# Optimization experiments

Measured on AMD Instinct MI355X. Metric: run time of the kernel, lower is better.

The kernel has to match this reference:

```python
import jax, jax.numpy as jnp
import numpy as np

EMB_DIM = 1024
NUM_HEADS = 16
SCALE_WEIGHTS = 1.0
TINY = jnp.finfo(jnp.float32).tiny


def setup_inputs() -> dict:
    key = jax.random.key(0)
    k1, k2, k3 = jax.random.split(key, 3)
    B, S = 2, 2048
    x = jax.random.normal(k1, (B, S, EMB_DIM), dtype=jnp.float32)
    weights = jax.random.uniform(k2, (B, S), dtype=jnp.float32)
    W_qkv = jax.random.normal(k3, (EMB_DIM, 3 * EMB_DIM), dtype=jnp.float32) / np.sqrt(EMB_DIM)
    b_qkv = jnp.zeros((3 * EMB_DIM,), dtype=jnp.float32)
    return {"x": x, "weights": weights, "W_qkv": W_qkv, "b_qkv": b_qkv}


def reference(x, weights, W_qkv, b_qkv):
    B, S, E = x.shape
    H = NUM_HEADS
    hd = E // H
    # QKV projection: [B,S,3E] -> [B,H,S,3*hd] -> split
    qkv = x @ W_qkv + b_qkv
    qkv = qkv.reshape(B, S, H, 3 * hd).transpose(0, 2, 1, 3)
    q, k, v = jnp.split(qkv, 3, axis=-1)  # each [B,H,S,hd]
    # weights: [B,S] -> [B,1,1,S] (broadcast over heads and query positions)
    w = weights[:, None, None, :]
    # scores with log-weight bias and hard masks
    attn_logits = jnp.einsum("bhqd,bhkd->bhqk", q, k) / jnp.sqrt(jnp.asarray(hd, x.dtype))
    attn_logits = attn_logits + jnp.log(w / SCALE_WEIGHTS + TINY)
    attn_logits = jnp.where(w == 0, -9e15, attn_logits)
    attn_logits = jnp.where(w == 1, 9e15, attn_logits)
    attention = jax.nn.softmax(attn_logits, axis=-1)
    values = jnp.einsum("bhqk,bhkd->bhqd", attention, v)
    return values.transpose(0, 2, 1, 3).reshape(B, S, E)
```

## Files before the change

### kernel.cpp

```cpp
#include <hip/hip_runtime.h>
#include <math.h>

#define B_  2
#define S_  2048
#define E_  1024
#define H_  16
#define HD_ 64
#define N3_ 3072
#define M_  (B_*S_)

typedef _Float16 h8 __attribute__((ext_vector_type(8)));
typedef _Float16 h4 __attribute__((ext_vector_type(4)));
typedef float    f4 __attribute__((ext_vector_type(4)));

__global__ void logw_kernel(const float* __restrict__ w, float* __restrict__ lw) {
    int i = blockIdx.x * blockDim.x + threadIdx.x;
    if (i < B_ * S_) {
        float x = w[i];
        float v;
        if (x == 0.0f)       v = -9.0e15f;
        else if (x == 1.0f)  v =  9.0e15f;
        else                 v = logf(x + 1.17549435e-38f);
        lw[i] = v;
    }
}

__global__ void cvt_x_kernel(const float* __restrict__ x, _Float16* __restrict__ x16) {
    int i = (blockIdx.x * 256 + threadIdx.x) * 8;
    float4 u = *(const float4*)&x[i];
    float4 v = *(const float4*)&x[i + 4];
    h8 o;
    o[0] = (_Float16)u.x; o[1] = (_Float16)u.y; o[2] = (_Float16)u.z; o[3] = (_Float16)u.w;
    o[4] = (_Float16)v.x; o[5] = (_Float16)v.y; o[6] = (_Float16)v.z; o[7] = (_Float16)v.w;
    *(h8*)&x16[i] = o;
}

__global__ __launch_bounds__(256) void transpose_w_kernel(
        const float* __restrict__ W, _Float16* __restrict__ Wt) {
    __shared__ float T[64][65];
    int k0 = blockIdx.x * 64, n0 = blockIdx.y * 64;
    int tid = threadIdx.x;
    int r = tid >> 4, c4 = (tid & 15) * 4;
#pragma unroll
    for (int i = 0; i < 4; i++) {
        int row = r + i * 16;
        float4 u = *(const float4*)&W[(size_t)(k0 + row) * N3_ + n0 + c4];
        T[c4 + 0][row] = u.x; T[c4 + 1][row] = u.y;
        T[c4 + 2][row] = u.z; T[c4 + 3][row] = u.w;
    }
    __syncthreads();
#pragma unroll
    for (int i = 0; i < 4; i++) {
        int rn = r + i * 16;
        h4 p;
        p[0] = (_Float16)T[rn][c4 + 0]; p[1] = (_Float16)T[rn][c4 + 1];
        p[2] = (_Float16)T[rn][c4 + 2]; p[3] = (_Float16)T[rn][c4 + 3];
        *(h4*)&Wt[(size_t)(n0 + rn) * E_ + k0 + c4] = p;
    }
}

__global__ __launch_bounds__(256) void qkv_gemm_f16(
        const _Float16* __restrict__ x16, const _Float16* __restrict__ wt,
        const float* __restrict__ bq,
        _Float16* __restrict__ qws, _Float16* __restrict__ kws,
        _Float16* __restrict__ vtws) {
    __shared__ _Float16 As[256 * 72];
    __shared__ _Float16 Ws[64 * 72];

    int tid = threadIdx.x;
    int wid = tid >> 6;
    int ln = tid & 15;
    int qd = (tid & 63) >> 4;
    int n0 = blockIdx.x * 64;
    int m0 = blockIdx.y * 256;
    int h = n0 / 192;
    int which = (n0 % 192) / 64;
    bool isV = (which == 2);

    f4 acc[4][4];
#pragma unroll
    for (int i = 0; i < 4; i++)
#pragma unroll
        for (int j = 0; j < 4; j++) acc[i][j] = (f4)0.0f;

    int sr = tid >> 3;
    int sc = (tid & 7) * 8;

    for (int k0 = 0; k0 < E_; k0 += 64) {
#pragma unroll
        for (int i = 0; i < 8; i++) {
            int row = sr + 32 * i;
            *(h8*)&As[row * 72 + sc] = *(const h8*)&x16[(size_t)(m0 + row) * E_ + k0 + sc];
        }
#pragma unroll
        for (int i = 0; i < 2; i++) {
            int row = sr + 32 * i;
            *(h8*)&Ws[row * 72 + sc] = *(const h8*)&wt[(size_t)(n0 + row) * E_ + k0 + sc];
        }
        __syncthreads();
#pragma unroll
        for (int ks = 0; ks < 2; ks++) {
            h8 a[4], b[4];
#pragma unroll
            for (int mt = 0; mt < 4; mt++)
                a[mt] = *(const h8*)&As[(wid * 64 + mt * 16 + ln) * 72 + ks * 32 + qd * 8];
#pragma unroll
            for (int nt = 0; nt < 4; nt++)
                b[nt] = *(const h8*)&Ws[(nt * 16 + ln) * 72 + ks * 32 + qd * 8];
            if (isV) {
#pragma unroll
                for (int i = 0; i < 4; i++)
#pragma unroll
                    for (int j = 0; j < 4; j++)
                        acc[i][j] = __builtin_amdgcn_mfma_f32_16x16x32_f16(a[i], b[j], acc[i][j], 0, 0, 0);
            } else {
#pragma unroll
                for (int i = 0; i < 4; i++)
#pragma unroll
                    for (int j = 0; j < 4; j++)
                        acc[i][j] = __builtin_amdgcn_mfma_f32_16x16x32_f16(b[i], a[j], acc[i][j], 0, 0, 0);
            }
        }
        __syncthreads();
    }

    int b = m0 >> 11;
    int bh = b * H_ + h;
    int sbase = (m0 & 2047) + wid * 64;

    if (isV) {
#pragma unroll
        for (int mt = 0; mt < 4; mt++) {
#pragma unroll
            for (int nt = 0; nt < 4; nt++) {
                int d = nt * 16 + ln;
                float bias = bq[n0 + nt * 16 + ln];
                f4 v = acc[mt][nt];
                h4 p;
                p[0] = (_Float16)(v[0] + bias); p[1] = (_Float16)(v[1] + bias);
                p[2] = (_Float16)(v[2] + bias); p[3] = (_Float16)(v[3] + bias);
                int s0 = sbase + mt * 16 + qd * 4;
                *(h4*)&vtws[((size_t)(bh * HD_ + d)) * S_ + s0] = p;
            }
        }
    } else {
        _Float16* dst = (which == 0) ? qws : kws;
        float scale = (which == 0) ? 0.125f : 1.0f;
#pragma unroll
        for (int nt = 0; nt < 4; nt++) {
            f4 bias4 = *(const f4*)&bq[n0 + nt * 16 + qd * 4];
#pragma unroll
            for (int mt = 0; mt < 4; mt++) {
                int s = sbase + mt * 16 + ln;
                f4 v = (acc[nt][mt] + bias4) * scale;
                h4 p;
                p[0] = (_Float16)v[0]; p[1] = (_Float16)v[1];
                p[2] = (_Float16)v[2]; p[3] = (_Float16)v[3];
                *(h4*)&dst[(((size_t)bh * S_ + s)) * HD_ + nt * 16 + qd * 4] = p;
            }
        }
    }
}

__global__ __launch_bounds__(256) void attn_kernel(
        const _Float16* __restrict__ q, const _Float16* __restrict__ k,
        const _Float16* __restrict__ vt, const float* __restrict__ lw,
        float* __restrict__ out) {
    __shared__ _Float16 Ks[64 * 72];
    __shared__ _Float16 Vts[64 * 72];
    __shared__ _Float16 Ps[128 * 72];
    __shared__ float lws[64];
    __shared__ float abuf[4][32];

    int tid = threadIdx.x;
    int wid = tid >> 6;
    int ln = tid & 15;
    int qd = (tid & 63) >> 4;
    int q0 = blockIdx.x * 128;
    int bh = blockIdx.y;
    int b = bh >> 4, h = bh & 15;

    const _Float16* qbase = q + (size_t)bh * S_ * HD_;
    const _Float16* kbase = k + (size_t)bh * S_ * HD_;
    const _Float16* vbase = vt + (size_t)bh * HD_ * S_;

    h8 qf[2][2];
#pragma unroll
    for (int qt = 0; qt < 2; qt++)
#pragma unroll
        for (int ds = 0; ds < 2; ds++)
            qf[qt][ds] = *(const h8*)&qbase[(size_t)(q0 + wid * 32 + qt * 16 + ln) * HD_ + ds * 32 + qd * 8];

    f4 o[2][4];
#pragma unroll
    for (int i = 0; i < 2; i++)
#pragma unroll
        for (int j = 0; j < 4; j++) o[i][j] = (f4)0.0f;
    float m_r[2] = {-INFINITY, -INFINITY};
    float l_r[2] = {0.0f, 0.0f};

    int sr = tid >> 3;
    int sc = (tid & 7) * 8;

    for (int kt = 0; kt < 32; kt++) {
        int k0 = kt * 64;
#pragma unroll
        for (int i = 0; i < 2; i++) {
            int row = sr + 32 * i;
            *(h8*)&Ks[row * 72 + sc]  = *(const h8*)&kbase[(size_t)(k0 + row) * HD_ + sc];
            *(h8*)&Vts[row * 72 + sc] = *(const h8*)&vbase[(size_t)row * S_ + k0 + sc];
        }
        if (tid < 64) lws[tid] = lw[b * S_ + k0 + tid];
        __syncthreads();

        f4 st[4][2];
#pragma unroll
        for (int i = 0; i < 4; i++)
#pragma unroll
            for (int j = 0; j < 2; j++) st[i][j] = (f4)0.0f;
#pragma unroll
        for (int ds = 0; ds < 2; ds++) {
            h8 kf[4];
#pragma unroll
            for (int i = 0; i < 4; i++)
                kf[i] = *(const h8*)&Ks[(i * 16 + ln) * 72 + ds * 32 + qd * 8];
#pragma unroll
            for (int i = 0; i < 4; i++)
#pragma unroll
                for (int qt = 0; qt < 2; qt++)
                    st[i][qt] = __builtin_amdgcn_mfma_f32_16x16x32_f16(kf[i], qf[qt][ds], st[i][qt], 0, 0, 0);
        }

        f4 lwv[4];
#pragma unroll
        for (int i = 0; i < 4; i++)
            lwv[i] = *(const f4*)&lws[i * 16 + qd * 4];
#pragma unroll
        for (int qt = 0; qt < 2; qt++) {
            float sv[16];
            float rm = -INFINITY;
#pragma unroll
            for (int i = 0; i < 4; i++)
#pragma unroll
                for (int r = 0; r < 4; r++) {
                    float v = st[i][qt][r] + lwv[i][r];
                    sv[i * 4 + r] = v;
                    rm = fmaxf(rm, v);
                }
            rm = fmaxf(rm, __shfl_xor(rm, 16));
            rm = fmaxf(rm, __shfl_xor(rm, 32));
            float mnew = fmaxf(m_r[qt], rm);
            float rs = 0.0f;
#pragma unroll
            for (int i = 0; i < 16; i++) {
                float e = __expf(sv[i] - mnew);
                sv[i] = e;
                rs += e;
            }
            rs += __shfl_xor(rs, 16);
            rs += __shfl_xor(rs, 32);
            float alpha = __expf(m_r[qt] - mnew);
            m_r[qt] = mnew;
            l_r[qt] = l_r[qt] * alpha + rs;
            if (qd == 0) abuf[wid][qt * 16 + ln] = alpha;
#pragma unroll
            for (int i = 0; i < 4; i++) {
                h4 p;
                p[0] = (_Float16)sv[i * 4 + 0]; p[1] = (_Float16)sv[i * 4 + 1];
                p[2] = (_Float16)sv[i * 4 + 2]; p[3] = (_Float16)sv[i * 4 + 3];
                *(h4*)&Ps[(wid * 32 + qt * 16 + ln) * 72 + i * 16 + qd * 4] = p;
            }
        }
        asm volatile("s_waitcnt lgkmcnt(0)" ::: "memory");

#pragma unroll
        for (int mt = 0; mt < 2; mt++) {
            f4 af = *(const f4*)&abuf[wid][mt * 16 + qd * 4];
#pragma unroll
            for (int nt = 0; nt < 4; nt++) o[mt][nt] *= af;
        }

#pragma unroll
        for (int ks = 0; ks < 2; ks++) {
            h8 pf[2], vf[4];
#pragma unroll
            for (int mt = 0; mt < 2; mt++)
                pf[mt] = *(const h8*)&Ps[(wid * 32 + mt * 16 + ln) * 72 + ks * 32 + qd * 8];
#pragma unroll
            for (int nt = 0; nt < 4; nt++)
                vf[nt] = *(const h8*)&Vts[(nt * 16 + ln) * 72 + ks * 32 + qd * 8];
#pragma unroll
            for (int mt = 0; mt < 2; mt++)
#pragma unroll
                for (int nt = 0; nt < 4; nt++)
                    o[mt][nt] = __builtin_amdgcn_mfma_f32_16x16x32_f16(pf[mt], vf[nt], o[mt][nt], 0, 0, 0);
        }
        __syncthreads();
    }

    if (qd == 0) {
        abuf[wid][ln] = l_r[0];
        abuf[wid][16 + ln] = l_r[1];
    }
    asm volatile("s_waitcnt lgkmcnt(0)" ::: "memory");
#pragma unroll
    for (int mt = 0; mt < 2; mt++) {
        f4 lf = *(const f4*)&abuf[wid][mt * 16 + qd * 4];
        f4 linv;
        linv[0] = 1.0f / lf[0]; linv[1] = 1.0f / lf[1];
        linv[2] = 1.0f / lf[2]; linv[3] = 1.0f / lf[3];
#pragma unroll
        for (int nt = 0; nt < 4; nt++) {
#pragma unroll
            for (int r = 0; r < 4; r++) {
                int s = q0 + wid * 32 + mt * 16 + qd * 4 + r;
                out[((size_t)(b * S_ + s)) * E_ + h * HD_ + nt * 16 + ln] = o[mt][nt][r] * linv[r];
            }
        }
    }
}

extern "C" void kernel_launch(void* const* d_in, const int* in_sizes, int n_in,
                              void* d_out, int out_size, void* d_ws, size_t ws_size,
                              hipStream_t stream) {
    const float* x  = (const float*)d_in[0];
    const float* w  = (const float*)d_in[1];
    const float* Wq = (const float*)d_in[2];
    const float* bq = (const float*)d_in[3];
    float* out = (float*)d_out;

    char* p = (char*)d_ws;
    _Float16* x16 = (_Float16*)p;              p += (size_t)M_ * E_ * 2;
    _Float16* wt  = (_Float16*)p;              p += (size_t)E_ * N3_ * 2;
    _Float16* qb  = (_Float16*)p;              p += (size_t)M_ * E_ * 2;
    _Float16* kb  = (_Float16*)p;              p += (size_t)M_ * E_ * 2;
    _Float16* vtb = (_Float16*)p;              p += (size_t)M_ * E_ * 2;
    float* lwb    = (float*)p;

    logw_kernel<<<dim3((B_ * S_ + 255) / 256), dim3(256), 0, stream>>>(w, lwb);
    cvt_x_kernel<<<dim3(M_ * E_ / 2048), dim3(256), 0, stream>>>(x, x16);
    transpose_w_kernel<<<dim3(E_ / 64, N3_ / 64), dim3(256), 0, stream>>>(Wq, wt);
    qkv_gemm_f16<<<dim3(N3_ / 64, M_ / 256), dim3(256), 0, stream>>>(x16, wt, bq, qb, kb, vtb);
    attn_kernel<<<dim3(S_ / 128, B_ * H_), dim3(256), 0, stream>>>(qb, kb, vtb, lwb, out);
}
```

Baseline: 211.0 us.

## Use direct global-to-LDS loads with XOR swizzle, exp2 softmax, smaller attention tiles

Both the QKV GEMM and attention kernel now stage tiles with global_load_lds (16-byte direct-to-LDS copies) into unpadded XOR-swizzled shared memory instead of register round-trips into padded arrays. Softmax moves to the base-2 domain: Q is prescaled by log2(e)/8, the log-weights use log2, and exp2 intrinsics replace expf, with the bias added by initialising the score accumulators. The attention kernel shrinks to 64 queries per block with a 1D remapped grid, launch_bounds occupancy 4, and the GEMM bias is folded into the accumulator init. The smaller tiles raise occupancy and parallelism but halve K/V reuse per block and increase total K/V traffic.

Measured after the change: 190.8 us. 9.6% less time.

```diff
diff --git a/kernel.cpp b/kernel.cpp
--- a/kernel.cpp
+++ b/kernel.cpp
@@ -13,6 +13,19 @@
 typedef _Float16 h4 __attribute__((ext_vector_type(4)));
 typedef float    f4 __attribute__((ext_vector_type(4)));
 
+typedef __attribute__((address_space(3))) unsigned int       lds_u32;
+typedef const __attribute__((address_space(1))) unsigned int glob_u32;
+
+__device__ __forceinline__ void gld16(const void* g, void* l) {
+    __builtin_amdgcn_global_load_lds((glob_u32*)g, (lds_u32*)l, 16, 0, 0);
+}
+
+__device__ __forceinline__ float exp2_hw(float x) {
+    return __builtin_amdgcn_exp2f(x);
+}
+
+#define QSCALE 0.18033688011112042f
+
 __global__ void logw_kernel(const float* __restrict__ w, float* __restrict__ lw) {
     int i = blockIdx.x * blockDim.x + threadIdx.x;
     if (i < B_ * S_) {
@@ -20,7 +33,7 @@
         float v;
         if (x == 0.0f)       v = -9.0e15f;
         else if (x == 1.0f)  v =  9.0e15f;
-        else                 v = logf(x + 1.17549435e-38f);
+        else                 v = log2f(x + 1.17549435e-38f);
         lw[i] = v;
     }
 }
@@ -64,49 +77,61 @@
         const float* __restrict__ bq,
         _Float16* __restrict__ qws, _Float16* __restrict__ kws,
         _Float16* __restrict__ vtws) {
-    __shared__ _Float16 As[256 * 72];
-    __shared__ _Float16 Ws[64 * 72];
+    __shared__ __align__(16) _Float16 As[256 * 64];
+    __shared__ __align__(16) _Float16 Ws[64 * 64];
 
     int tid = threadIdx.x;
-    int wid = tid >> 6;
-    int ln = tid & 15;
-    int qd = (tid & 63) >> 4;
+    int wid = tid >> 6, lane = tid & 63;
+    int ln = tid & 15, qd = lane >> 4;
     int n0 = blockIdx.x * 64;
     int m0 = blockIdx.y * 256;
     int h = n0 / 192;
     int which = (n0 % 192) / 64;
     bool isV = (which == 2);
 
+    int srow = lane >> 3;
+    int schunk = (lane & 7) ^ srow;
+
     f4 acc[4][4];
-#pragma unroll
-    for (int i = 0; i < 4; i++)
-#pragma unroll
-        for (int j = 0; j < 4; j++) acc[i][j] = (f4)0.0f;
-
-    int sr = tid >> 3;
-    int sc = (tid & 7) * 8;
+    if (isV) {
+#pragma unroll
+        for (int nt = 0; nt < 4; nt++) {
+            float bv = bq[n0 + nt * 16 + ln];
+            f4 b4; b4[0] = bv; b4[1] = bv; b4[2] = bv; b4[3] = bv;
+#pragma unroll
+            for (int mt = 0; mt < 4; mt++) acc[mt][nt] = b4;
+        }
+    } else {
+#pragma unroll
+        for (int nt = 0; nt < 4; nt++) {
+            f4 b4 = *(const f4*)&bq[n0 + nt * 16 + qd * 4];
+#pragma unroll
+            for (int mt = 0; mt < 4; mt++) acc[nt][mt] = b4;
+        }
+    }
+
+    const _Float16* agp = &x16[(size_t)(m0 + wid * 64 + srow) * E_ + schunk * 8];
+    const _Float16* wgp = &wt[(size_t)(n0 + wid * 16 + srow) * E_ + schunk * 8];
+    int sw = ln & 7;
 
     for (int k0 = 0; k0 < E_; k0 += 64) {
 #pragma unroll
-        for (int i = 0; i < 8; i++) {
-            int row = sr + 32 * i;
-            *(h8*)&As[row * 72 + sc] = *(const h8*)&x16[(size_t)(m0 + row) * E_ + k0 + sc];
-        }
-#pragma unroll
-        for (int i = 0; i < 2; i++) {
-            int row = sr + 32 * i;
-            *(h8*)&Ws[row * 72 + sc] = *(const h8*)&wt[(size_t)(n0 + row) * E_ + k0 + sc];
-        }
+        for (int j = 0; j < 8; j++)
+            gld16(agp + (size_t)j * 8 * E_ + k0, &As[(wid * 64 + j * 8) * 64]);
+#pragma unroll
+        for (int j = 0; j < 2; j++)
+            gld16(wgp + (size_t)j * 8 * E_ + k0, &Ws[(wid * 16 + j * 8) * 64]);
         __syncthreads();
 #pragma unroll
         for (int ks = 0; ks < 2; ks++) {
+            int ch = ((ks * 4 + qd) ^ sw) * 8;
             h8 a[4], b[4];
 #pragma unroll
             for (int mt = 0; mt < 4; mt++)
-                a[mt] = *(const h8*)&As[(wid * 64 + mt * 16 + ln) * 72 + ks * 32 + qd * 8];
+                a[mt] = *(const h8*)&As[(wid * 64 + mt * 16 + ln) * 64 + ch];
 #pragma unroll
             for (int nt = 0; nt < 4; nt++)
-                b[nt] = *(const h8*)&Ws[(nt * 16 + ln) * 72 + ks * 32 + qd * 8];
+                b[nt] = *(const h8*)&Ws[(nt * 16 + ln) * 64 + ch];
             if (isV) {
 #pragma unroll
                 for (int i = 0; i < 4; i++)
@@ -130,194 +155,159 @@
 
     if (isV) {
 #pragma unroll
-        for (int mt = 0; mt < 4; mt++) {
+        for (int mt = 0; mt < 4; mt++)
 #pragma unroll
             for (int nt = 0; nt < 4; nt++) {
-                int d = nt * 16 + ln;
-                float bias = bq[n0 + nt * 16 + ln];
                 f4 v = acc[mt][nt];
-                h4 p;
-                p[0] = (_Float16)(v[0] + bias); p[1] = (_Float16)(v[1] + bias);
-                p[2] = (_Float16)(v[2] + bias); p[3] = (_Float16)(v[3] + bias);
-                int s0 = sbase + mt * 16 + qd * 4;
-                *(h4*)&vtws[((size_t)(bh * HD_ + d)) * S_ + s0] = p;
-            }
-        }
-    } else {
-        _Float16* dst = (which == 0) ? qws : kws;
-        float scale = (which == 0) ? 0.125f : 1.0f;
-#pragma unroll
-        for (int nt = 0; nt < 4; nt++) {
-            f4 bias4 = *(const f4*)&bq[n0 + nt * 16 + qd * 4];
-#pragma unroll
-            for (int mt = 0; mt < 4; mt++) {
-                int s = sbase + mt * 16 + ln;
-                f4 v = (acc[nt][mt] + bias4) * scale;
                 h4 p;
                 p[0] = (_Float16)v[0]; p[1] = (_Float16)v[1];
                 p[2] = (_Float16)v[2]; p[3] = (_Float16)v[3];
-                *(h4*)&dst[(((size_t)bh * S_ + s)) * HD_ + nt * 16 + qd * 4] = p;
+                *(h4*)&vtws[((size_t)(bh * HD_ + nt * 16 + ln)) * S_ + sbase + mt * 16 + qd * 4] = p;
             }
-        }
-    }
-}
-
-__global__ __launch_bounds__(256) void attn_kernel(
+    } else {
+        _Float16* dst = (which == 0) ? qws : kws;
+        float scale = (which == 0) ? QSCALE : 1.0f;
+#pragma unroll
+        for (int nt = 0; nt < 4; nt++)
+#pragma unroll
+            for (int mt = 0; mt < 4; mt++) {
+                f4 v = acc[nt][mt] * scale;
+                h4 p;
+                p[0] = (_Float16)v[0]; p[1] = (_Float16)v[1];
+                p[2] = (_Float16)v[2]; p[3] = (_Float16)v[3];
+                *(h4*)&dst[(((size_t)bh * S_ + sbase + mt * 16 + ln)) * HD_ + nt * 16 + qd * 4] = p;
+            }
+    }
+}
+
+__global__ __launch_bounds__(256, 4) void attn_kernel(
         const _Float16* __restrict__ q, const _Float16* __restrict__ k,
         const _Float16* __restrict__ vt, const float* __restrict__ lw,
         float* __restrict__ out) {
-    __shared__ _Float16 Ks[64 * 72];
-    __shared__ _Float16 Vts[64 * 72];
-    __shared__ _Float16 Ps[128 * 72];
+    __shared__ __align__(16) _Float16 Ks[64 * 64];
+    __shared__ __align__(16) _Float16 Vts[64 * 64];
+    __shared__ __align__(16) _Float16 Ps[64 * 72];
     __shared__ float lws[64];
-    __shared__ float abuf[4][32];
+    __shared__ float abuf[4][16];
 
     int tid = threadIdx.x;
-    int wid = tid >> 6;
-    int ln = tid & 15;
-    int qd = (tid & 63) >> 4;
-    int q0 = blockIdx.x * 128;
-    int bh = blockIdx.y;
+    int wid = tid >> 6, lane = tid & 63;
+    int ln = tid & 15, qd = lane >> 4;
+    int L = blockIdx.x;
+    int sl = L >> 3;
+    int bh = (L & 7) + 8 * (sl >> 5);
+    int q0 = (sl & 31) * 64;
     int b = bh >> 4, h = bh & 15;
 
     const _Float16* qbase = q + (size_t)bh * S_ * HD_;
     const _Float16* kbase = k + (size_t)bh * S_ * HD_;
     const _Float16* vbase = vt + (size_t)bh * HD_ * S_;
 
-    h8 qf[2][2];
-#pragma unroll
-    for (int qt = 0; qt < 2; qt++)
-#pragma unroll
-        for (int ds = 0; ds < 2; ds++)
-            qf[qt][ds] = *(const h8*)&qbase[(size_t)(q0 + wid * 32 + qt * 16 + ln) * HD_ + ds * 32 + qd * 8];
-
-    f4 o[2][4];
-#pragma unroll
-    for (int i = 0; i < 2; i++)
-#pragma unroll
-        for (int j = 0; j < 4; j++) o[i][j] = (f4)0.0f;
-    float m_r[2] = {-INFINITY, -INFINITY};
-    float l_r[2] = {0.0f, 0.0f};
-
-    int sr = tid >> 3;
-    int sc = (tid & 7) * 8;
+    int srow = lane >> 3;
+    int schunk = (lane & 7) ^ srow;
+    int sw = ln & 7;
+
+    h8 qf[2];
+#pragma unroll
+    for (int ds = 0; ds < 2; ds++)
+        qf[ds] = *(const h8*)&qbase[(size_t)(q0 + wid * 16 + ln) * HD_ + ds * 32 + qd * 8];
+
+    f4 o[4];
+#pragma unroll
+    for (int j = 0; j < 4; j++) o[j] = (f4)0.0f;
+    float m_r = -INFINITY, l_r = 0.0f;
+
+    const _Float16* kgp = &kbase[(size_t)(wid * 16 + srow) * HD_ + schunk * 8];
+    const _Float16* vgp = &vbase[(size_t)(wid * 16 + srow) * S_ + schunk * 8];
 
     for (int kt = 0; kt < 32; kt++) {
         int k0 = kt * 64;
 #pragma unroll
-        for (int i = 0; i < 2; i++) {
-            int row = sr + 32 * i;
-            *(h8*)&Ks[row * 72 + sc]  = *(const h8*)&kbase[(size_t)(k0 + row) * HD_ + sc];
-            *(h8*)&Vts[row * 72 + sc] = *(const h8*)&vbase[(size_t)row * S_ + k0 + sc];
+        for (int j = 0; j < 2; j++) {
+            gld16(kgp + (size_t)(k0 + j * 8) * HD_, &Ks[(wid * 16 + j * 8) * 64]);
+            gld16(vgp + (size_t)j * 8 * S_ + k0, &Vts[(wid * 16 + j * 8) * 64]);
         }
         if (tid < 64) lws[tid] = lw[b * S_ + k0 + tid];
         __syncthreads();
 
-        f4 st[4][2];
+        f4 st[4];
+#pragma unroll
+        for (int i = 0; i < 4; i++) st[i] = *(const f4*)&lws[i * 16 + qd * 4];
+#pragma unroll
+        for (int ds = 0; ds < 2; ds++) {
+            int ch = ((ds * 4 + qd) ^ sw) * 8;
+            h8 kf[4];
+#pragma unroll
+            for (int i = 0; i < 4; i++)
+                kf[i] = *(const h8*)&Ks[(i * 16 + ln) * 64 + ch];
+#pragma unroll
+            for (int i = 0; i < 4; i++)
+                st[i] = __builtin_amdgcn_mfma_f32_16x16x32_f16(kf[i], qf[ds], st[i], 0, 0, 0);
+        }
+
+        float rm = -INFINITY;
 #pragma unroll
         for (int i = 0; i < 4; i++)
 #pragma unroll
-            for (int j = 0; j < 2; j++) st[i][j] = (f4)0.0f;
-#pragma unroll
-        for (int ds = 0; ds < 2; ds++) {
-            h8 kf[4];
-#pragma unroll
-            for (int i = 0; i < 4; i++)
-                kf[i] = *(const h8*)&Ks[(i * 16 + ln) * 72 + ds * 32 + qd * 8];
-#pragma unroll
-            for (int i = 0; i < 4; i++)
-#pragma unroll
-                for (int qt = 0; qt < 2; qt++)
-                    st[i][qt] = __builtin_amdgcn_mfma_f32_16x16x32_f16(kf[i], qf[qt][ds], st[i][qt], 0, 0, 0);
-        }
-
-        f4 lwv[4];
+            for (int r = 0; r < 4; r++) rm = fmaxf(rm, st[i][r]);
+        rm = fmaxf(rm, __shfl_xor(rm, 16));
+        rm = fmaxf(rm, __shfl_xor(rm, 32));
+        float mnew = fmaxf(m_r, rm);
+        float rs = 0.0f;
 #pragma unroll
         for (int i = 0; i < 4; i++)
-            lwv[i] = *(const f4*)&lws[i * 16 + qd * 4];
-#pragma unroll
-        for (int qt = 0; qt < 2; qt++) {
-            float sv[16];
-            float rm = -INFINITY;
-#pragma unroll
-            for (int i = 0; i < 4; i++)
-#pragma unroll
-                for (int r = 0; r < 4; r++) {
-                    float v = st[i][qt][r] + lwv[i][r];
-                    sv[i * 4 + r] = v;
-                    rm = fmaxf(rm, v);
-                }
-            rm = fmaxf(rm, __shfl_xor(rm, 16));
-            rm = fmaxf(rm, __shfl_xor(rm, 32));
-            float mnew = fmaxf(m_r[qt], rm);
-            float rs = 0.0f;
-#pragma unroll
-            for (int i = 0; i < 16; i++) {
-                float e = __expf(sv[i] - mnew);
-                sv[i] = e;
+#pragma unroll
+            for (int r = 0; r < 4; r++) {
+                float e = exp2_hw(st[i][r] - mnew);
+                st[i][r] = e;
                 rs += e;
             }
-            rs += __shfl_xor(rs, 16);
-            rs += __shfl_xor(rs, 32);
-            float alpha = __expf(m_r[qt] - mnew);
-            m_r[qt] = mnew;
-            l_r[qt] = l_r[qt] * alpha + rs;
-            if (qd == 0) abuf[wid][qt * 16 + ln] = alpha;
-#pragma unroll
-            for (int i = 0; i < 4; i++) {
-                h4 p;
-                p[0] = (_Float16)sv[i * 4 + 0]; p[1] = (_Float16)sv[i * 4 + 1];
-                p[2] = (_Float16)sv[i * 4 + 2]; p[3] = (_Float16)sv[i * 4 + 3];
-                *(h4*)&Ps[(wid * 32 + qt * 16 + ln) * 72 + i * 16 + qd * 4] = p;
-            }
+        rs += __shfl_xor(rs, 16);
+        rs += __shfl_xor(rs, 32);
+        float alpha = exp2_hw(m_r - mnew);
+        m_r = mnew;
+        l_r = l_r * alpha + rs;
+        if (qd == 0) abuf[wid][ln] = alpha;
+#pragma unroll
+        for (int i = 0; i < 4; i++) {
+            h4 p;
+            p[0] = (_Float16)st[i][0]; p[1] = (_Float16)st[i][1];
+            p[2] = (_Float16)st[i][2]; p[3] = (_Float16)st[i][3];
+            *(h4*)&Ps[(wid * 16 + ln) * 72 + i * 16 + qd * 4] = p;
         }
         asm volatile("s_waitcnt lgkmcnt(0)" ::: "memory");
 
-#pragma unroll
-        for (int mt = 0; mt < 2; mt++) {
-            f4 af = *(const f4*)&abuf[wid][mt * 16 + qd * 4];
-#pragma unroll
-            for (int nt = 0; nt < 4; nt++) o[mt][nt] *= af;
-        }
+        f4 af = *(const f4*)&abuf[wid][qd * 4];
+#pragma unroll
+        for (int nt = 0; nt < 4; nt++) o[nt] *= af;
 
 #pragma unroll
         for (int ks = 0; ks < 2; ks++) {
-            h8 pf[2], vf[4];
-#pragma unroll
-            for (int mt = 0; mt < 2; mt++)
-                pf[mt] = *(const h8*)&Ps[(wid * 32 + mt * 16 + ln) * 72 + ks * 32 + qd * 8];
+            int ch = ((ks * 4 + qd) ^ sw) * 8;
+            h8 pf = *(const h8*)&Ps[(wid * 16 + ln) * 72 + ks * 32 + qd * 8];
+            h8 vf[4];
 #pragma unroll
             for (int nt = 0; nt < 4; nt++)
-                vf[nt] = *(const h8*)&Vts[(nt * 16 + ln) * 72 + ks * 32 + qd * 8];
-#pragma unroll
-            for (int mt = 0; mt < 2; mt++)
-#pragma unroll
-                for (int nt = 0; nt < 4; nt++)
-                    o[mt][nt] = __builtin_amdgcn_mfma_f32_16x16x32_f16(pf[mt], vf[nt], o[mt][nt], 0, 0, 0);
+                vf[nt] = *(const h8*)&Vts[(nt * 16 + ln) * 64 + ch];
+#pragma unroll
+            for (int nt = 0; nt < 4; nt++)
+                o[nt] = __builtin_amdgcn_mfma_f32_16x16x32_f16(pf, vf[nt], o[nt], 0, 0, 0);
         }
         __syncthreads();
     }
 
-    if (qd == 0) {
-        abuf[wid][ln] = l_r[0];
-        abuf[wid][16 + ln] = l_r[1];
-    }
+    if (qd == 0) abuf[wid][ln] = l_r;
     asm volatile("s_waitcnt lgkmcnt(0)" ::: "memory");
-#pragma unroll
-    for (int mt = 0; mt < 2; mt++) {
-        f4 lf = *(const f4*)&abuf[wid][mt * 16 + qd * 4];
-        f4 linv;
-        linv[0] = 1.0f / lf[0]; linv[1] = 1.0f / lf[1];
-        linv[2] = 1.0f / lf[2]; linv[3] = 1.0f / lf[3];
-#pragma unroll
-        for (int nt = 0; nt < 4; nt++) {
-#pragma unroll
-            for (int r = 0; r < 4; r++) {
-                int s = q0 + wid * 32 + mt * 16 + qd * 4 + r;
-                out[((size_t)(b * S_ + s)) * E_ + h * HD_ + nt * 16 + ln] = o[mt][nt][r] * linv[r];
-            }
-        }
-    }
+    f4 lf = *(const f4*)&abuf[wid][qd * 4];
+    f4 linv;
+    linv[0] = 1.0f / lf[0]; linv[1] = 1.0f / lf[1];
+    linv[2] = 1.0f / lf[2]; linv[3] = 1.0f / lf[3];
+    float* obase = &out[((size_t)(b * S_ + q0 + wid * 16 + qd * 4)) * E_ + h * HD_];
+#pragma unroll
+    for (int nt = 0; nt < 4; nt++)
+#pragma unroll
+        for (int r = 0; r < 4; r++)
+            obase[(size_t)r * E_ + nt * 16 + ln] = o[nt][r] * linv[r];
 }
 
 extern "C" void kernel_launch(void* const* d_in, const int* in_sizes, int n_in,
@@ -341,5 +331,5 @@
     cvt_x_kernel<<<dim3(M_ * E_ / 2048), dim3(256), 0, stream>>>(x, x16);
     transpose_w_kernel<<<dim3(E_ / 64, N3_ / 64), dim3(256), 0, stream>>>(Wq, wt);
     qkv_gemm_f16<<<dim3(N3_ / 64, M_ / 256), dim3(256), 0, stream>>>(x16, wt, bq, qb, kb, vtb);
-    attn_kernel<<<dim3(S_ / 128, B_ * H_), dim3(256), 0, stream>>>(qb, kb, vtb, lwb, out);
-}
+    attn_kernel<<<dim3(S_ / 64 * B_ * H_), dim3(256), 0, stream>>>(qb, kb, vtb, lwb, out);
+}
```
